# Performance work log

Measured on AMD Instinct MI355X. Metric: run time of the kernel, lower is better.

Reference implementation:

```python
import jax, jax.numpy as jnp
import numpy as np

NORM_EPS = 1e-6
QK_SCALE = 1.0 / 128.0  # 1/d_head (muP)
ROTARY_BASE = 10000
INFTY_APPROX = 1e30

B, T, M, H, D = 2, 2048, 1024, 8, 128


def _rmsnorm(x, eps=NORM_EPS):
    # normalize over the last (head) dim; no learned gains (norm_gains=False)
    ms = jnp.mean(jnp.square(x), axis=-1, keepdims=True)
    return x / jnp.sqrt(ms + eps)


def _rope(x, base=ROTARY_BASE):
    # x: [b, h, t, d]; rotate (even-half, odd-half) pairs as in the source
    length, width = x.shape[-2], x.shape[-1]
    half = width // 2
    pos = jnp.arange(length, dtype=x.dtype)[:, None]            # [t, 1]
    freqs = jnp.power(jnp.asarray(base, x.dtype), -jnp.arange(half, dtype=x.dtype) / half)[None, :]
    rad = pos * freqs                                            # [t, half]
    cos = jnp.cos(rad)[None, None]
    sin = jnp.sin(rad)[None, None]
    even, odd = jnp.split(x, 2, axis=-1)
    return jnp.concatenate([even * cos - odd * sin, even * sin + odd * cos], axis=-1)


def setup_inputs() -> dict:
    key = jax.random.key(0)
    ks = jax.random.split(key, 5)
    std = M ** -0.5
    return {
        "x": jax.random.normal(ks[0], (B, T, M), jnp.float32),
        "wq": jax.random.normal(ks[1], (M, H, D), jnp.float32) * std,
        "wk": jax.random.normal(ks[2], (M, H, D), jnp.float32) * std,
        "wv": jax.random.normal(ks[3], (M, H, D), jnp.float32) * std,
        "wo": jax.random.normal(ks[4], (H, D, M), jnp.float32) * std,
    }


def reference(x, wq, wk, wv, wo):
    # projections: [b, h, t, d]
    q = jnp.einsum('bim,mhd->bhid', x, wq)
    k = jnp.einsum('bim,mhd->bhid', x, wk)
    v = jnp.einsum('bim,mhd->bhid', x, wv)
    # qk RMSNorm (norm_gains=False)
    q = _rmsnorm(q)
    k = _rmsnorm(k)
    # inline RoPE
    q = _rope(q)
    k = _rope(k)
    # scaled scores: mult applied to both q and k (mult^2 = qk_scale)
    mult = jnp.asarray(QK_SCALE ** 0.5, q.dtype)
    s = jnp.einsum('bhid,bhjd->bhij', q * mult, k * mult)
    # causal mask: subtract large constant where i < j
    t = s.shape[-1]
    mask = (jnp.arange(t)[:, None] < jnp.arange(t)[None, :]).astype(s.dtype)
    s = s - jnp.asarray(INFTY_APPROX, s.dtype) * mask[None, None]
    p = jax.nn.softmax(s, axis=-1)
    o = jnp.einsum('bhij,bhjd->bhid', p, v)
    return jnp.einsum('bhid,hdm->bim', o, wo)
```

## Files before the change

### kernel.cpp

```cpp
#include <hip/hip_runtime.h>
#include <hip/hip_bf16.h>
#include <math.h>

#define B_  2
#define T_  2048
#define M_  1024
#define H_  8
#define D_  128
#define NROW (B_ * T_)
#define HD  (H_ * D_)

#define NORM_EPS 1e-6f
#define QK_MULT  0.08838834764831845f
#define ROT_BASE 10000.0f

typedef short bf16x8 __attribute__((ext_vector_type(8)));
typedef float f32x4  __attribute__((ext_vector_type(4)));

static __device__ __forceinline__ unsigned short f2bf(float f) {
    union { __hip_bfloat16 h; unsigned short u; } cv;
    cv.h = __float2bfloat16(f);
    return cv.u;
}
static __device__ __forceinline__ float bf2f(unsigned short u) {
    union { unsigned short u; __hip_bfloat16 h; } cv;
    cv.u = u;
    return __bfloat162float(cv.h);
}

static __device__ __forceinline__ void gload_lds16(const unsigned short* g,
                                                   unsigned short* l) {
    __builtin_amdgcn_global_load_lds(
        (const __attribute__((address_space(1))) void*)g,
        (__attribute__((address_space(3))) void*)l, 16, 0, 0);
}

__global__ __launch_bounds__(256) void cast_bf16(const float* __restrict__ in,
                                                 unsigned short* __restrict__ out)
{
    const int i = (blockIdx.x * 256 + threadIdx.x) * 4;
    const float4 v = *(const float4*)(in + i);
    ushort4 o;
    o.x = f2bf(v.x); o.y = f2bf(v.y); o.z = f2bf(v.z); o.w = f2bf(v.w);
    *(ushort4*)(out + i) = o;
}

__global__ __launch_bounds__(256) void transpose_cast4(const float* __restrict__ w0,
                                                       const float* __restrict__ w1,
                                                       const float* __restrict__ w2,
                                                       const float* __restrict__ w3,
                                                       unsigned short* __restrict__ wqkvT,
                                                       unsigned short* __restrict__ woT)
{
    __shared__ float t[32][33];
    const int z = blockIdx.z;
    const float* in = z == 0 ? w0 : (z == 1 ? w1 : (z == 2 ? w2 : w3));
    unsigned short* out = z < 3 ? (wqkvT + (size_t)z * 1024 * 1024) : woT;

    const int tx = threadIdx.x & 31;
    const int ty = threadIdx.x >> 5;
    const int n0 = blockIdx.x * 32;
    const int k0 = blockIdx.y * 32;
    #pragma unroll
    for (int r = 0; r < 4; ++r)
        t[ty + r * 8][tx] = in[(size_t)(k0 + ty + r * 8) * 1024 + n0 + tx];
    __syncthreads();
    #pragma unroll
    for (int r = 0; r < 4; ++r)
        out[(size_t)(n0 + ty + r * 8) * 1024 + k0 + tx] = f2bf(t[tx][ty + r * 8]);
}

__global__ __launch_bounds__(256) void v_transpose(const unsigned short* __restrict__ vb,
                                                   unsigned short* __restrict__ vt)
{
    __shared__ unsigned short s[32][33];
    const int tx = threadIdx.x & 31;
    const int ty = threadIdx.x >> 5;
    const int t0 = blockIdx.x * 32;
    const int d0 = blockIdx.y * 32;
    const int bh = blockIdx.z;
    const int h = bh & 7, b = bh >> 3;

    #pragma unroll
    for (int r = 0; r < 4; ++r)
        s[ty + r * 8][tx] = vb[(size_t)(b * T_ + t0 + ty + r * 8) * 1024 + h * 128 + d0 + tx];
    __syncthreads();
    #pragma unroll
    for (int r = 0; r < 4; ++r)
        vt[((size_t)bh * 128 + d0 + ty + r * 8) * T_ + t0 + tx] = s[tx][ty + r * 8];
}

template <int MODE>
__global__ __launch_bounds__(256) void gemm_bt(const unsigned short* __restrict__ A,
                                               const unsigned short* __restrict__ Bt,
                                               unsigned short* __restrict__ oq,
                                               unsigned short* __restrict__ ok,
                                               unsigned short* __restrict__ ov,
                                               float* __restrict__ cf)
{
    __shared__ unsigned short As[128 * 32];
    __shared__ unsigned short Bs[128 * 32];

    const int tid  = threadIdx.x;
    const int lane = tid & 63;
    const int w    = tid >> 6;
    const int g    = lane >> 4;
    const int lc   = lane & 15;
    const int wm   = w >> 1;
    const int wn   = w & 1;

    const int m0 = blockIdx.y * 128;
    const int n0 = blockIdx.x * 128;

    const unsigned short* aBase = A  + (size_t)m0 * 1024;
    const unsigned short* bBase = Bt + (size_t)n0 * 1024;

    f32x4 acc[4][4];
    #pragma unroll
    for (int i = 0; i < 4; ++i)
        #pragma unroll
        for (int j = 0; j < 4; ++j)
            acc[i][j] = (f32x4){0.f, 0.f, 0.f, 0.f};

    for (int kt = 0; kt < 32; ++kt) {
        const int k0 = kt * 32;
        #pragma unroll
        for (int it = 0; it < 2; ++it) {
            const int u  = tid + it * 256;
            const int r2 = u >> 2;
            const int s2 = u & 3;
            gload_lds16(aBase + (size_t)r2 * 1024 + k0 + s2 * 8, &As[u * 8]);
            gload_lds16(bBase + (size_t)r2 * 1024 + k0 + s2 * 8, &Bs[u * 8]);
        }
        __syncthreads();

        bf16x8 af[4], bfr[4];
        #pragma unroll
        for (int i = 0; i < 4; ++i)
            af[i] = *(const bf16x8*)&As[(wm * 64 + i * 16 + lc) * 32 + g * 8];
        #pragma unroll
        for (int j = 0; j < 4; ++j)
            bfr[j] = *(const bf16x8*)&Bs[(wn * 64 + j * 16 + lc) * 32 + g * 8];

        #pragma unroll
        for (int i = 0; i < 4; ++i)
            #pragma unroll
            for (int j = 0; j < 4; ++j)
                acc[i][j] = __builtin_amdgcn_mfma_f32_16x16x32_bf16(af[i], bfr[j], acc[i][j], 0, 0, 0);
        __syncthreads();
    }

    if (MODE == 0) {
        const int which = n0 >> 10;
        unsigned short* outp = which == 0 ? oq : (which == 1 ? ok : ov);
        const int ncol0 = (n0 & 1023) + wn * 64;
        #pragma unroll
        for (int i = 0; i < 4; ++i) {
            const int mrow = m0 + wm * 64 + i * 16 + g * 4;
            #pragma unroll
            for (int j = 0; j < 4; ++j) {
                const int nc = ncol0 + j * 16 + lc;
                #pragma unroll
                for (int r = 0; r < 4; ++r)
                    outp[(size_t)(mrow + r) * 1024 + nc] = f2bf(acc[i][j][r]);
            }
        }
    } else {
        #pragma unroll
        for (int i = 0; i < 4; ++i) {
            const int mrow = m0 + wm * 64 + i * 16 + g * 4;
            #pragma unroll
            for (int j = 0; j < 4; ++j) {
                const int nc = n0 + wn * 64 + j * 16 + lc;
                #pragma unroll
                for (int r = 0; r < 4; ++r)
                    cf[(size_t)(mrow + r) * 1024 + nc] = acc[i][j][r];
            }
        }
    }
}

__global__ __launch_bounds__(256) void rmsnorm_rope_bf16(unsigned short* __restrict__ q,
                                                         unsigned short* __restrict__ k)
{
    const int vec = blockIdx.x * 4 + (threadIdx.x >> 6);
    unsigned short* p = (blockIdx.y == 0 ? q : k) + (size_t)vec * 128;
    const int t = (vec / H_) % T_;
    const int lane = threadIdx.x & 63;

    float e = bf2f(p[lane]);
    float o = bf2f(p[lane + 64]);
    float ss = e * e + o * o;
    #pragma unroll
    for (int off = 32; off; off >>= 1) ss += __shfl_xor(ss, off);
    const float r = rsqrtf(ss * (1.0f / 128.0f) + NORM_EPS) * QK_MULT;
    e *= r;
    o *= r;

    const float freq = expf(-(float)lane * (logf(ROT_BASE) / 64.0f));
    const float rad = (float)t * freq;
    const float c = cosf(rad);
    const float s = sinf(rad);

    p[lane]      = f2bf(e * c - o * s);
    p[lane + 64] = f2bf(e * s + o * c);
}

#define PLD 72

__global__ __launch_bounds__(256) void flash_attn(const unsigned short* __restrict__ qb,
                                                  const unsigned short* __restrict__ kb,
                                                  const unsigned short* __restrict__ vt,
                                                  unsigned short* __restrict__ o)
{
    __shared__ unsigned short Ks[2][64 * 128];
    __shared__ unsigned short Vs[2][128 * 64];
    __shared__ unsigned short Ps[4][16 * PLD];

    const int tid  = threadIdx.x;
    const int lane = tid & 63;
    const int w    = tid >> 6;
    const int g    = lane >> 4;
    const int lc   = lane & 15;

    const int bh = blockIdx.x;
    const int h  = bh & (H_ - 1);
    const int b  = bh >> 3;
    const int yy = blockIdx.y;
    const int qt = (yy & 1) ? (31 - (yy >> 1)) : (yy >> 1);
    const int q0 = qt * 64;

    const size_t bhbase  = (size_t)b * T_ * HD + (size_t)h * 128;
    const size_t bhvbase = (size_t)bh * 128 * T_;

    int mI[4];
    size_t srcKoff[4], srcVoff[4];
    #pragma unroll
    for (int it = 0; it < 4; ++it) {
        const int m = (w * 4 + it) * 64 + lane;
        mI[it] = m;
        const int jK = m >> 4, cK = (m & 15) ^ (jK & 15);
        srcKoff[it] = (size_t)jK * 1024 + cK * 8;
        const int dV = m >> 3, cV = (m & 7) ^ (dV & 7);
        srcVoff[it] = (size_t)dV * T_ + cV * 8;
    }
    const unsigned short* kgb = kb + bhbase;
    const unsigned short* vgb = vt + bhvbase;

    bf16x8 qf[4];
    {
        const unsigned short* qp = qb + bhbase + (size_t)(q0 + w * 16 + lc) * 1024 + g * 8;
        #pragma unroll
        for (int dc = 0; dc < 4; ++dc)
            qf[dc] = *(const bf16x8*)(qp + dc * 32);
    }

    float lsum[4] = {0.f, 0.f, 0.f, 0.f};
    f32x4 oacc[8];
    #pragma unroll
    for (int dc8 = 0; dc8 < 8; ++dc8) oacc[dc8] = (f32x4){0.f, 0.f, 0.f, 0.f};

    #pragma unroll
    for (int it = 0; it < 4; ++it) {
        gload_lds16(kgb + srcKoff[it], &Ks[0][mI[it] * 8]);
        gload_lds16(vgb + srcVoff[it], &Vs[0][mI[it] * 8]);
    }

    for (int jt = 0; jt <= qt; ++jt) {
        const int cur = jt & 1;
        __syncthreads();

        if (jt < qt) {
            const size_t j0n = (size_t)(jt + 1) * 64;
            #pragma unroll
            for (int it = 0; it < 4; ++it) {
                gload_lds16(kgb + j0n * 1024 + srcKoff[it], &Ks[cur ^ 1][mI[it] * 8]);
                gload_lds16(vgb + j0n + srcVoff[it], &Vs[cur ^ 1][mI[it] * 8]);
            }
        }

        f32x4 sacc[4];
        #pragma unroll
        for (int jc = 0; jc < 4; ++jc) {
            sacc[jc] = (f32x4){0.f, 0.f, 0.f, 0.f};
            #pragma unroll
            for (int dc = 0; dc < 4; ++dc) {
                bf16x8 bf = *(const bf16x8*)&Ks[cur][(jc * 16 + lc) * 128 + (((dc * 4 + g) ^ lc) << 3)];
                sacc[jc] = __builtin_amdgcn_mfma_f32_16x16x32_bf16(qf[dc], bf, sacc[jc], 0, 0, 0);
            }
        }

        if (jt == qt) {
            const int qi = q0 + w * 16 + g * 4;
            #pragma unroll
            for (int jc = 0; jc < 4; ++jc) {
                const int jj = q0 + jc * 16 + lc;
                #pragma unroll
                for (int r = 0; r < 4; ++r)
                    if (qi + r < jj) sacc[jc][r] = -1e30f;
            }
        }

        #pragma unroll
        for (int jc = 0; jc < 4; ++jc)
            #pragma unroll
            for (int r = 0; r < 4; ++r) {
                const float p = __expf(sacc[jc][r]);
                sacc[jc][r] = p;
                lsum[r] += p;
            }

        unsigned short* pw = Ps[w];
        #pragma unroll
        for (int jc = 0; jc < 4; ++jc)
            #pragma unroll
            for (int r = 0; r < 4; ++r)
                pw[(g * 4 + r) * PLD + jc * 16 + lc] = f2bf(sacc[jc][r]);

        __asm__ volatile("s_waitcnt lgkmcnt(0)" ::: "memory");

        bf16x8 pa[2];
        #pragma unroll
        for (int jc2 = 0; jc2 < 2; ++jc2)
            pa[jc2] = *(const bf16x8*)&pw[lc * PLD + jc2 * 32 + g * 8];

        #pragma unroll
        for (int dc8 = 0; dc8 < 8; ++dc8) {
            #pragma unroll
            for (int jc2 = 0; jc2 < 2; ++jc2) {
                bf16x8 bv = *(const bf16x8*)&Vs[cur][(dc8 * 16 + lc) * 64 + (((jc2 * 4 + g) ^ (lc & 7)) << 3)];
                oacc[dc8] = __builtin_amdgcn_mfma_f32_16x16x32_bf16(pa[jc2], bv, oacc[dc8], 0, 0, 0);
            }
        }
    }

    #pragma unroll
    for (int r = 0; r < 4; ++r) {
        float l = lsum[r];
        #pragma unroll
        for (int off = 1; off < 16; off <<= 1) l += __shfl_xor(l, off);
        const float inv = 1.0f / l;
        unsigned short* op = o + bhbase + (size_t)(q0 + w * 16 + g * 4 + r) * 1024 + lc;
        #pragma unroll
        for (int dc8 = 0; dc8 < 8; ++dc8)
            op[dc8 * 16] = f2bf(oacc[dc8][r] * inv);
    }
}

extern "C" void kernel_launch(void* const* d_in, const int* in_sizes, int n_in,
                              void* d_out, int out_size, void* d_ws, size_t ws_size,
                              hipStream_t stream)
{
    const float* x  = (const float*)d_in[0];
    const float* wq = (const float*)d_in[1];
    const float* wk = (const float*)d_in[2];
    const float* wv = (const float*)d_in[3];
    const float* wo = (const float*)d_in[4];
    float* out = (float*)d_out;

    const size_t SZ = (size_t)NROW * HD;
    unsigned short* qb    = (unsigned short*)d_ws;
    unsigned short* kb    = qb + SZ;
    unsigned short* vb    = kb + SZ;
    unsigned short* ob    = vb + SZ;
    unsigned short* xb    = ob + SZ;
    unsigned short* vt    = xb + SZ;
    unsigned short* wqkvT = vt + SZ;
    unsigned short* woT   = wqkvT + 3 * 1024 * 1024;

    cast_bf16<<<SZ / (256 * 4), 256, 0, stream>>>(x, xb);
    transpose_cast4<<<dim3(32, 32, 4), 256, 0, stream>>>(wq, wk, wv, wo, wqkvT, woT);

    gemm_bt<0><<<dim3(24, 32), 256, 0, stream>>>(xb, wqkvT, qb, kb, vb, nullptr);

    v_transpose<<<dim3(64, 4, 16), 256, 0, stream>>>(vb, vt);

    rmsnorm_rope_bf16<<<dim3(NROW * H_ / 4, 2), 256, 0, stream>>>(qb, kb);

    flash_attn<<<dim3(B_ * H_, 32), 256, 0, stream>>>(qb, kb, vt, ob);

    gemm_bt<1><<<dim3(8, 32), 256, 0, stream>>>(ob, woT, nullptr, nullptr, nullptr, out);
}
```

Before: 209.2 us.

## Fuse V transpose into QKV GEMM and restructure flash attention with 32x32 MFMA

The QKV projection epilogue now writes V directly in transposed [b,h,d,t] layout, which removes the separate v_transpose kernel and its extra round trip through global memory. The flash attention kernel switches to 32x32x16 MFMA and computes S transposed (K times Q), so P can be assembled in registers with a cross-lane shuffle instead of being staged through LDS. The key dimension of each tile is split across wave pairs, fully masked diagonal sub-tiles are skipped, and the two partial outputs are merged through shared memory at the end. The price is more accumulator registers per thread, which may lower occupancy, plus a final reduction step through shared memory.

Result: slower. 214.6 us (+2.6%).

```diff
diff --git a/kernel.cpp b/kernel.cpp
--- a/kernel.cpp
+++ b/kernel.cpp
@@ -14,8 +14,9 @@
 #define QK_MULT  0.08838834764831845f
 #define ROT_BASE 10000.0f
 
-typedef short bf16x8 __attribute__((ext_vector_type(8)));
-typedef float f32x4  __attribute__((ext_vector_type(4)));
+typedef short bf16x8  __attribute__((ext_vector_type(8)));
+typedef float f32x4   __attribute__((ext_vector_type(4)));
+typedef float f32x16  __attribute__((ext_vector_type(16)));
 
 static __device__ __forceinline__ unsigned short f2bf(float f) {
     union { __hip_bfloat16 h; unsigned short u; } cv;
@@ -26,6 +27,9 @@
     union { unsigned short u; __hip_bfloat16 h; } cv;
     cv.u = u;
     return __bfloat162float(cv.h);
+}
+static __device__ __forceinline__ unsigned int pk2bf(float a, float b) {
+    return ((unsigned int)f2bf(b) << 16) | f2bf(a);
 }
 
 static __device__ __forceinline__ void gload_lds16(const unsigned short* g,
@@ -70,32 +74,12 @@
         out[(size_t)(n0 + ty + r * 8) * 1024 + k0 + tx] = f2bf(t[tx][ty + r * 8]);
 }
 
-__global__ __launch_bounds__(256) void v_transpose(const unsigned short* __restrict__ vb,
-                                                   unsigned short* __restrict__ vt)
-{
-    __shared__ unsigned short s[32][33];
-    const int tx = threadIdx.x & 31;
-    const int ty = threadIdx.x >> 5;
-    const int t0 = blockIdx.x * 32;
-    const int d0 = blockIdx.y * 32;
-    const int bh = blockIdx.z;
-    const int h = bh & 7, b = bh >> 3;
-
-    #pragma unroll
-    for (int r = 0; r < 4; ++r)
-        s[ty + r * 8][tx] = vb[(size_t)(b * T_ + t0 + ty + r * 8) * 1024 + h * 128 + d0 + tx];
-    __syncthreads();
-    #pragma unroll
-    for (int r = 0; r < 4; ++r)
-        vt[((size_t)bh * 128 + d0 + ty + r * 8) * T_ + t0 + tx] = s[tx][ty + r * 8];
-}
-
 template <int MODE>
 __global__ __launch_bounds__(256) void gemm_bt(const unsigned short* __restrict__ A,
                                                const unsigned short* __restrict__ Bt,
                                                unsigned short* __restrict__ oq,
                                                unsigned short* __restrict__ ok,
-                                               unsigned short* __restrict__ ov,
+                                               unsigned short* __restrict__ vt,
                                                float* __restrict__ cf)
 {
     __shared__ unsigned short As[128 * 32];
@@ -152,17 +136,34 @@
 
     if (MODE == 0) {
         const int which = n0 >> 10;
-        unsigned short* outp = which == 0 ? oq : (which == 1 ? ok : ov);
         const int ncol0 = (n0 & 1023) + wn * 64;
-        #pragma unroll
-        for (int i = 0; i < 4; ++i) {
-            const int mrow = m0 + wm * 64 + i * 16 + g * 4;
-            #pragma unroll
-            for (int j = 0; j < 4; ++j) {
-                const int nc = ncol0 + j * 16 + lc;
+        if (which < 2) {
+            unsigned short* outp = which == 0 ? oq : ok;
+            #pragma unroll
+            for (int i = 0; i < 4; ++i) {
+                const int mrow = m0 + wm * 64 + i * 16 + g * 4;
                 #pragma unroll
-                for (int r = 0; r < 4; ++r)
-                    outp[(size_t)(mrow + r) * 1024 + nc] = f2bf(acc[i][j][r]);
+                for (int j = 0; j < 4; ++j) {
+                    const int nc = ncol0 + j * 16 + lc;
+                    #pragma unroll
+                    for (int r = 0; r < 4; ++r)
+                        outp[(size_t)(mrow + r) * 1024 + nc] = f2bf(acc[i][j][r]);
+                }
+            }
+        } else {
+            const int b2 = m0 >> 11;
+            #pragma unroll
+            for (int i = 0; i < 4; ++i) {
+                const int t = (m0 & 2047) + wm * 64 + i * 16 + g * 4;
+                #pragma unroll
+                for (int j = 0; j < 4; ++j) {
+                    const int nc = ncol0 + j * 16 + lc;
+                    const int hh = nc >> 7, dd = nc & 127;
+                    uint2 val;
+                    val.x = pk2bf(acc[i][j][0], acc[i][j][1]);
+                    val.y = pk2bf(acc[i][j][2], acc[i][j][3]);
+                    *(uint2*)(vt + (((size_t)(b2 * 8 + hh) * 128 + dd) * T_ + t)) = val;
+                }
             }
         }
     } else {
@@ -206,22 +207,24 @@
     p[lane + 64] = f2bf(e * s + o * c);
 }
 
-#define PLD 72
-
 __global__ __launch_bounds__(256) void flash_attn(const unsigned short* __restrict__ qb,
                                                   const unsigned short* __restrict__ kb,
                                                   const unsigned short* __restrict__ vt,
                                                   unsigned short* __restrict__ o)
 {
-    __shared__ unsigned short Ks[2][64 * 128];
-    __shared__ unsigned short Vs[2][128 * 64];
-    __shared__ unsigned short Ps[4][16 * PLD];
+    __shared__ __align__(16) unsigned short smem[2 * 64 * 128 + 2 * 128 * 64 + 128];
+    unsigned short* KsB = smem;
+    unsigned short* VsB = smem + 2 * 64 * 128;
+    float* lscr = (float*)(smem + 2 * 64 * 128 + 2 * 128 * 64);
+    float* scr  = (float*)smem;
 
     const int tid  = threadIdx.x;
     const int lane = tid & 63;
     const int w    = tid >> 6;
-    const int g    = lane >> 4;
-    const int lc   = lane & 15;
+    const int wj   = w >> 1;
+    const int wq2  = w & 1;
+    const int qcol = lane & 31;
+    const int hi   = lane >> 5;
 
     const int bh = blockIdx.x;
     const int h  = bh & (H_ - 1);
@@ -247,103 +250,129 @@
     const unsigned short* kgb = kb + bhbase;
     const unsigned short* vgb = vt + bhvbase;
 
-    bf16x8 qf[4];
+    bf16x8 qf[8];
     {
-        const unsigned short* qp = qb + bhbase + (size_t)(q0 + w * 16 + lc) * 1024 + g * 8;
-        #pragma unroll
-        for (int dc = 0; dc < 4; ++dc)
-            qf[dc] = *(const bf16x8*)(qp + dc * 32);
-    }
-
-    float lsum[4] = {0.f, 0.f, 0.f, 0.f};
-    f32x4 oacc[8];
-    #pragma unroll
-    for (int dc8 = 0; dc8 < 8; ++dc8) oacc[dc8] = (f32x4){0.f, 0.f, 0.f, 0.f};
+        const unsigned short* qp = qb + bhbase + (size_t)(q0 + wq2 * 32 + qcol) * 1024 + hi * 8;
+        #pragma unroll
+        for (int ks = 0; ks < 8; ++ks)
+            qf[ks] = *(const bf16x8*)(qp + ks * 16);
+    }
+
+    float lsum = 0.f;
+    f32x16 otacc[4];
+    #pragma unroll
+    for (int dch = 0; dch < 4; ++dch)
+        #pragma unroll
+        for (int r = 0; r < 16; ++r) otacc[dch][r] = 0.f;
 
     #pragma unroll
     for (int it = 0; it < 4; ++it) {
-        gload_lds16(kgb + srcKoff[it], &Ks[0][mI[it] * 8]);
-        gload_lds16(vgb + srcVoff[it], &Vs[0][mI[it] * 8]);
+        gload_lds16(kgb + srcKoff[it], &KsB[mI[it] * 8]);
+        gload_lds16(vgb + srcVoff[it], &VsB[mI[it] * 8]);
     }
 
     for (int jt = 0; jt <= qt; ++jt) {
         const int cur = jt & 1;
+        unsigned short* Ks = KsB + cur * (64 * 128);
+        unsigned short* Vs = VsB + cur * (128 * 64);
         __syncthreads();
 
         if (jt < qt) {
             const size_t j0n = (size_t)(jt + 1) * 64;
+            unsigned short* Kn = KsB + (cur ^ 1) * (64 * 128);
+            unsigned short* Vn = VsB + (cur ^ 1) * (128 * 64);
             #pragma unroll
             for (int it = 0; it < 4; ++it) {
-                gload_lds16(kgb + j0n * 1024 + srcKoff[it], &Ks[cur ^ 1][mI[it] * 8]);
-                gload_lds16(vgb + j0n + srcVoff[it], &Vs[cur ^ 1][mI[it] * 8]);
-            }
-        }
-
-        f32x4 sacc[4];
-        #pragma unroll
-        for (int jc = 0; jc < 4; ++jc) {
-            sacc[jc] = (f32x4){0.f, 0.f, 0.f, 0.f};
-            #pragma unroll
-            for (int dc = 0; dc < 4; ++dc) {
-                bf16x8 bf = *(const bf16x8*)&Ks[cur][(jc * 16 + lc) * 128 + (((dc * 4 + g) ^ lc) << 3)];
-                sacc[jc] = __builtin_amdgcn_mfma_f32_16x16x32_bf16(qf[dc], bf, sacc[jc], 0, 0, 0);
-            }
-        }
-
-        if (jt == qt) {
-            const int qi = q0 + w * 16 + g * 4;
-            #pragma unroll
-            for (int jc = 0; jc < 4; ++jc) {
-                const int jj = q0 + jc * 16 + lc;
+                gload_lds16(kgb + j0n * 1024 + srcKoff[it], &Kn[mI[it] * 8]);
+                gload_lds16(vgb + j0n + srcVoff[it], &Vn[mI[it] * 8]);
+            }
+        }
+
+        const bool dead = (jt == qt) && (wj > wq2);
+        if (!dead) {
+            f32x16 sacc;
+            #pragma unroll
+            for (int r = 0; r < 16; ++r) sacc[r] = 0.f;
+            const int jrow = wj * 32 + qcol;
+            #pragma unroll
+            for (int ks = 0; ks < 8; ++ks) {
+                const int c = ks * 2 + hi;
+                bf16x8 af = *(const bf16x8*)&Ks[(jrow * 16 + (c ^ (lane & 15))) * 8];
+                sacc = __builtin_amdgcn_mfma_f32_32x32x16_bf16(af, qf[ks], sacc, 0, 0, 0);
+            }
+
+            if (jt == qt && wj == wq2) {
                 #pragma unroll
-                for (int r = 0; r < 4; ++r)
-                    if (qi + r < jj) sacc[jc][r] = -1e30f;
-            }
-        }
-
-        #pragma unroll
-        for (int jc = 0; jc < 4; ++jc)
-            #pragma unroll
-            for (int r = 0; r < 4; ++r) {
-                const float p = __expf(sacc[jc][r]);
-                sacc[jc][r] = p;
-                lsum[r] += p;
-            }
-
-        unsigned short* pw = Ps[w];
-        #pragma unroll
-        for (int jc = 0; jc < 4; ++jc)
-            #pragma unroll
-            for (int r = 0; r < 4; ++r)
-                pw[(g * 4 + r) * PLD + jc * 16 + lc] = f2bf(sacc[jc][r]);
-
-        __asm__ volatile("s_waitcnt lgkmcnt(0)" ::: "memory");
-
-        bf16x8 pa[2];
-        #pragma unroll
-        for (int jc2 = 0; jc2 < 2; ++jc2)
-            pa[jc2] = *(const bf16x8*)&pw[lc * PLD + jc2 * 32 + g * 8];
-
-        #pragma unroll
-        for (int dc8 = 0; dc8 < 8; ++dc8) {
-            #pragma unroll
-            for (int jc2 = 0; jc2 < 2; ++jc2) {
-                bf16x8 bv = *(const bf16x8*)&Vs[cur][(dc8 * 16 + lc) * 64 + (((jc2 * 4 + g) ^ (lc & 7)) << 3)];
-                oacc[dc8] = __builtin_amdgcn_mfma_f32_16x16x32_bf16(pa[jc2], bv, oacc[dc8], 0, 0, 0);
-            }
-        }
-    }
-
-    #pragma unroll
-    for (int r = 0; r < 4; ++r) {
-        float l = lsum[r];
-        #pragma unroll
-        for (int off = 1; off < 16; off <<= 1) l += __shfl_xor(l, off);
+                for (int r = 0; r < 16; ++r) {
+                    const int jl = (r & 3) + 8 * (r >> 2) + 4 * hi;
+                    if (qcol < jl) sacc[r] = -1e30f;
+                }
+            }
+
+            unsigned int dw[8];
+            #pragma unroll
+            for (int m2 = 0; m2 < 8; ++m2) {
+                const float p0 = __expf(sacc[2 * m2]);
+                const float p1 = __expf(sacc[2 * m2 + 1]);
+                lsum += p0 + p1;
+                dw[m2] = pk2bf(p0, p1);
+            }
+            unsigned int ex[8];
+            #pragma unroll
+            for (int m2 = 0; m2 < 8; ++m2)
+                ex[m2] = (unsigned int)__shfl_xor((int)dw[m2], 32);
+
+            #pragma unroll
+            for (int ks2 = 0; ks2 < 2; ++ks2) {
+                union { unsigned int u[4]; bf16x8 v; } pf;
+                pf.u[0] = hi ? ex[4 * ks2 + 2] : dw[4 * ks2 + 0];
+                pf.u[1] = hi ? ex[4 * ks2 + 3] : dw[4 * ks2 + 1];
+                pf.u[2] = hi ? dw[4 * ks2 + 2] : ex[4 * ks2 + 0];
+                pf.u[3] = hi ? dw[4 * ks2 + 3] : ex[4 * ks2 + 1];
+                #pragma unroll
+                for (int dch = 0; dch < 4; ++dch) {
+                    const int c = wj * 4 + ks2 * 2 + hi;
+                    const int drow = dch * 32 + qcol;
+                    bf16x8 af = *(const bf16x8*)&Vs[(drow * 8 + (c ^ (lane & 7))) * 8];
+                    otacc[dch] = __builtin_amdgcn_mfma_f32_32x32x16_bf16(af, pf.v, otacc[dch], 0, 0, 0);
+                }
+            }
+        }
+    }
+
+    lsum += __shfl_xor(lsum, 32);
+    __syncthreads();
+
+    if (wj == 1) {
+        float* s0 = scr + (size_t)(wq2 * 32 + qcol) * 129;
+        #pragma unroll
+        for (int dch = 0; dch < 4; ++dch)
+            #pragma unroll
+            for (int r = 0; r < 16; ++r)
+                s0[dch * 32 + (r & 3) + 8 * (r >> 2) + 4 * hi] = otacc[dch][r];
+        if (hi == 0) lscr[wq2 * 32 + qcol] = lsum;
+    }
+    __syncthreads();
+    if (wj == 0) {
+        const float l = lsum + lscr[wq2 * 32 + qcol];
         const float inv = 1.0f / l;
-        unsigned short* op = o + bhbase + (size_t)(q0 + w * 16 + g * 4 + r) * 1024 + lc;
-        #pragma unroll
-        for (int dc8 = 0; dc8 < 8; ++dc8)
-            op[dc8 * 16] = f2bf(oacc[dc8][r] * inv);
+        const float* s0 = scr + (size_t)(wq2 * 32 + qcol) * 129;
+        unsigned short* op = o + bhbase + (size_t)(q0 + wq2 * 32 + qcol) * 1024;
+        #pragma unroll
+        for (int dch = 0; dch < 4; ++dch) {
+            #pragma unroll
+            for (int k4 = 0; k4 < 4; ++k4) {
+                const int d0 = dch * 32 + 8 * k4 + 4 * hi;
+                const float f0 = (otacc[dch][4 * k4 + 0] + s0[d0 + 0]) * inv;
+                const float f1 = (otacc[dch][4 * k4 + 1] + s0[d0 + 1]) * inv;
+                const float f2 = (otacc[dch][4 * k4 + 2] + s0[d0 + 2]) * inv;
+                const float f3 = (otacc[dch][4 * k4 + 3] + s0[d0 + 3]) * inv;
+                uint2 val;
+                val.x = pk2bf(f0, f1);
+                val.y = pk2bf(f2, f3);
+                *(uint2*)(op + d0) = val;
+            }
+        }
     }
 }
 
@@ -361,19 +390,16 @@
     const size_t SZ = (size_t)NROW * HD;
     unsigned short* qb    = (unsigned short*)d_ws;
     unsigned short* kb    = qb + SZ;
-    unsigned short* vb    = kb + SZ;
-    unsigned short* ob    = vb + SZ;
+    unsigned short* vt    = kb + SZ;
+    unsigned short* ob    = vt + SZ;
     unsigned short* xb    = ob + SZ;
-    unsigned short* vt    = xb + SZ;
-    unsigned short* wqkvT = vt + SZ;
+    unsigned short* wqkvT = xb + SZ;
     unsigned short* woT   = wqkvT + 3 * 1024 * 1024;
 
     cast_bf16<<<SZ / (256 * 4), 256, 0, stream>>>(x, xb);
     transpose_cast4<<<dim3(32, 32, 4), 256, 0, stream>>>(wq, wk, wv, wo, wqkvT, woT);
 
-    gemm_bt<0><<<dim3(24, 32), 256, 0, stream>>>(xb, wqkvT, qb, kb, vb, nullptr);
-
-    v_transpose<<<dim3(64, 4, 16), 256, 0, stream>>>(vb, vt);
+    gemm_bt<0><<<dim3(24, 32), 256, 0, stream>>>(xb, wqkvT, qb, kb, vt, nullptr);
 
     rmsnorm_rope_bf16<<<dim3(NROW * H_ / 4, 2), 256, 0, stream>>>(qb, kb);
 
```
